# Performance work log

Measured on AMD Instinct MI355X. Metric: run time of the kernel, lower is better.

## Reference

```python
import jax, jax.numpy as jnp
import numpy as np

D_MODEL = 768
N_HEADS = 12
D_K = D_MODEL // N_HEADS
NEG_INF = -1e9


def setup_inputs() -> dict:
    key = jax.random.key(0)
    ks = jax.random.split(key, 7)
    B, S = 4, 2048
    x = jax.random.normal(ks[0], (B, S, D_MODEL), dtype=jnp.float32)
    # causal mask, broadcastable to [B, H, S, S]
    mask = jnp.tril(jnp.ones((S, S), dtype=bool))[None, None, :, :]
    scale = 1.0 / np.sqrt(D_MODEL)
    Wq = jax.random.normal(ks[1], (D_MODEL, D_MODEL), dtype=jnp.float32) * scale
    bq = jnp.zeros((D_MODEL,), dtype=jnp.float32)
    Wk = jax.random.normal(ks[2], (D_MODEL, D_MODEL), dtype=jnp.float32) * scale
    bk = jnp.zeros((D_MODEL,), dtype=jnp.float32)
    Wv = jax.random.normal(ks[3], (D_MODEL, D_MODEL), dtype=jnp.float32) * scale
    bv = jnp.zeros((D_MODEL,), dtype=jnp.float32)
    return {"x": x, "mask": mask, "Wq": Wq, "bq": bq, "Wk": Wk, "bk": bk, "Wv": Wv, "bv": bv}


def reference(x, mask, Wq, bq, Wk, bk, Wv, bv):
    B, S, _ = x.shape
    # projections (torch Linear: y = x @ W.T + b)
    q = (x @ Wq.T + bq).reshape(B, S, N_HEADS, D_K)
    k = (x @ Wk.T + bk).reshape(B, S, N_HEADS, D_K)
    v = (x @ Wv.T + bv).reshape(B, S, N_HEADS, D_K)
    # scores: [B, H, S, S]
    scores = jnp.einsum("bqhd,bkhd->bhqk", q, k) / jnp.sqrt(jnp.float32(D_K))
    scores = jnp.where(mask, scores, NEG_INF)
    probs = jax.nn.softmax(scores, axis=-1)
    # attention: [B, H, S, D_K] -> [B, S, d_model]
    attn = jnp.einsum("bhqk,bkhd->bqhd", probs, v).reshape(B, S, D_MODEL)
    return attn
```

## Files before the change

### kernel.cpp

```cpp
#include <hip/hip_runtime.h>
#include <math.h>


#define S_LEN 2048
#define BATCH 4
#define HEADS 12
#define DM 768
#define DK 64
#define BH (BATCH*HEADS)
#define MROWS (BATCH*S_LEN)
#define QSCALE 0.1803368801111244f

typedef __attribute__((ext_vector_type(8))) short short8;
typedef __attribute__((ext_vector_type(4))) float floatx4;
typedef __attribute__((ext_vector_type(16))) float floatx16;
typedef __attribute__((ext_vector_type(4))) unsigned int uintx4;
typedef __attribute__((address_space(3))) unsigned char lds_byte;
typedef __attribute__((address_space(1))) const unsigned char glob_byte;

__device__ __forceinline__ unsigned short f2bf(float f) {
  union { float f; unsigned int u; } a; a.f = f;
  unsigned int u = a.u;
  return (unsigned short)((u + 0x7fffu + ((u >> 16) & 1u)) >> 16);
}

__global__ void cast_f32_bf16(const float* __restrict__ src,
                              unsigned short* __restrict__ dst, int n) {
  int i = (blockIdx.x * blockDim.x + threadIdx.x) * 4;
  if (i < n) {
    float4 v = *(const float4*)(src + i);
    ushort4 o;
    o.x = f2bf(v.x); o.y = f2bf(v.y); o.z = f2bf(v.z); o.w = f2bf(v.w);
    *(ushort4*)(dst + i) = o;
  }
}

__global__ void cast_w3(const float* __restrict__ w0, const float* __restrict__ w1,
                        const float* __restrict__ w2, unsigned short* __restrict__ dst,
                        int n) {
  const float* src = (blockIdx.y == 0) ? w0 : (blockIdx.y == 1) ? w1 : w2;
  int i = (blockIdx.x * blockDim.x + threadIdx.x) * 4;
  if (i < n) {
    float4 v = *(const float4*)(src + i);
    ushort4 o;
    o.x = f2bf(v.x); o.y = f2bf(v.y); o.z = f2bf(v.z); o.w = f2bf(v.w);
    *(ushort4*)(dst + (size_t)blockIdx.y * n + i) = o;
  }
}

__global__ __launch_bounds__(256) void qkv_gemm(
    const unsigned short* __restrict__ xb,
    const unsigned short* __restrict__ wb,
    const float* __restrict__ bq, const float* __restrict__ bk,
    const float* __restrict__ bv,
    unsigned short* __restrict__ qo,
    unsigned short* __restrict__ ko,
    unsigned short* __restrict__ vto) {
  __shared__ unsigned short a_lds[2 * 128 * 32];
  __shared__ unsigned short b_lds[2 * 128 * 32];
  const int mat = blockIdx.z;
  const int tid = threadIdx.x;
  const int wave = tid >> 6, lane = tid & 63, quad = lane >> 4, ln = lane & 15;
  const int wm = wave & 1, wn = wave >> 1;
  const int m_blk = blockIdx.x * 128, n_blk = blockIdx.y * 128;
  const unsigned short* w = wb + (size_t)mat * DM * DM;
  const int srow_i[2] = { (0 * 256 + wave * 64 + lane) >> 2,
                          (1 * 256 + wave * 64 + lane) >> 2 };
  const int sq = (lane & 3) * 8;

  const floatx4 fz = {0.f, 0.f, 0.f, 0.f};
  floatx4 acc[4][4];
#pragma unroll
  for (int mg = 0; mg < 4; mg++)
#pragma unroll
    for (int c = 0; c < 4; c++) acc[mg][c] = fz;

  for (int k0 = 0; k0 < DM; k0 += 64) {
#pragma unroll
    for (int p = 0; p < 2; p++)
#pragma unroll
      for (int i = 0; i < 2; i++) {
        const int cbase = i * 256 + wave * 64;
        const int row = srow_i[i];
        __builtin_amdgcn_global_load_lds(
            (glob_byte*)(xb + (size_t)(m_blk + row) * DM + k0 + p * 32 + sq),
            (lds_byte*)(a_lds + p * 4096 + cbase * 8), 16, 0, 0);
        __builtin_amdgcn_global_load_lds(
            (glob_byte*)(w + (size_t)(n_blk + row) * DM + k0 + p * 32 + sq),
            (lds_byte*)(b_lds + p * 4096 + cbase * 8), 16, 0, 0);
      }
    __syncthreads();

    short8 af[4][2], bf[4][2];
#pragma unroll
    for (int mg = 0; mg < 4; mg++)
#pragma unroll
      for (int p = 0; p < 2; p++)
        af[mg][p] = *(const short8*)(a_lds + p * 4096 + (wm * 64 + mg * 16 + ln) * 32 + quad * 8);
#pragma unroll
    for (int c = 0; c < 4; c++)
#pragma unroll
      for (int p = 0; p < 2; p++)
        bf[c][p] = *(const short8*)(b_lds + p * 4096 + (wn * 64 + c * 16 + ln) * 32 + quad * 8);
#pragma unroll
    for (int mg = 0; mg < 4; mg++)
#pragma unroll
      for (int c = 0; c < 4; c++) {
        acc[mg][c] = __builtin_amdgcn_mfma_f32_16x16x32_bf16(af[mg][0], bf[c][0], acc[mg][c], 0, 0, 0);
        acc[mg][c] = __builtin_amdgcn_mfma_f32_16x16x32_bf16(af[mg][1], bf[c][1], acc[mg][c], 0, 0, 0);
      }
    __syncthreads();
  }

  const float* bias = (mat == 0) ? bq : (mat == 1) ? bk : bv;
  const float oscale = (mat == 0) ? QSCALE : 1.0f;
  const int m_base = m_blk + wm * 64, n_base = n_blk + wn * 64;
#pragma unroll
  for (int mg = 0; mg < 4; mg++)
#pragma unroll
    for (int c = 0; c < 4; c++) {
      int gn = n_base + c * 16 + ln;
      int hd = gn >> 6, d = gn & 63;
      float bias_v = bias[gn] * oscale;
      int gm0 = m_base + mg * 16 + quad * 4;
      int bb = gm0 >> 11, s0 = gm0 & (S_LEN - 1);
      if (mat == 2) {
        ushort4 pk;
        pk.x = f2bf(acc[mg][c][0] + bias_v);
        pk.y = f2bf(acc[mg][c][1] + bias_v);
        pk.z = f2bf(acc[mg][c][2] + bias_v);
        pk.w = f2bf(acc[mg][c][3] + bias_v);
        *(ushort4*)(vto + (((size_t)(bb * HEADS + hd)) * DK + d) * S_LEN + s0) = pk;
      } else {
        unsigned short* dst = (mat == 0 ? qo : ko) +
            (((size_t)(bb * HEADS + hd)) * S_LEN + s0) * DK + d;
#pragma unroll
        for (int r = 0; r < 4; r++)
          dst[(size_t)r * DK] = f2bf(acc[mg][c][r] * oscale + bias_v);
      }
    }
}

__global__ __launch_bounds__(128) void flash_attn(
    const unsigned short* __restrict__ q,
    const unsigned short* __restrict__ k,
    const unsigned short* __restrict__ vt,
    float* __restrict__ out) {
  const int id = blockIdx.x;
  const int bh = id % BH;
  const int qt = (S_LEN / 64 - 1) - (id / BH);
  const int q0 = qt * 64;
  const int tid = threadIdx.x;
  const int wave = tid >> 6, lane = tid & 63;
  const int l31 = lane & 31, hi = lane >> 5;
  const unsigned short* qp = q  + (size_t)bh * S_LEN * DK;
  const unsigned short* kp = k  + (size_t)bh * S_LEN * DK;
  const unsigned short* vp = vt + (size_t)bh * DK * S_LEN;
  const int qr_base = q0 + wave * 32;

  const floatx16 fz16 = {0.f,0.f,0.f,0.f,0.f,0.f,0.f,0.f,
                         0.f,0.f,0.f,0.f,0.f,0.f,0.f,0.f};

  short8 ones;
#pragma unroll
  for (int j = 0; j < 8; j++) ones[j] = (short)0x3F80;

  short8 aq[4];
#pragma unroll
  for (int ks = 0; ks < 4; ks++)
    aq[ks] = *(const short8*)(qp + (size_t)(qr_base + l31) * DK + ks * 16 + hi * 8);

  floatx16 o0 = fz16, o1 = fz16, lacc = fz16;

  auto loadK = [&](int k0, short8 (&kf)[2][4]) {
#pragma unroll
    for (int kg = 0; kg < 2; kg++)
#pragma unroll
      for (int ks = 0; ks < 4; ks++)
        kf[kg][ks] = *(const short8*)(kp + (size_t)(k0 + kg * 32 + l31) * DK + ks * 16 + hi * 8);
  };

  auto body = [&](int k0, short8 (&kf)[2][4]) {
    short8 vf[2][2][2];
#pragma unroll
    for (int dg = 0; dg < 2; dg++)
#pragma unroll
      for (int kg = 0; kg < 2; kg++)
#pragma unroll
        for (int ks2 = 0; ks2 < 2; ks2++)
          vf[dg][kg][ks2] = *(const short8*)(vp + (size_t)(dg * 32 + l31) * S_LEN
                                             + k0 + kg * 32 + ks2 * 16 + hi * 8);
    const bool domask = (k0 + 63 > qr_base);
#pragma unroll
    for (int kg = 0; kg < 2; kg++) {
      floatx16 sc = fz16;
#pragma unroll
      for (int ks = 0; ks < 4; ks++)
        sc = __builtin_amdgcn_mfma_f32_32x32x16_bf16(kf[kg][ks], aq[ks], sc, 0, 0, 0);
      float pv[16];
      const int qr = qr_base + l31;
#pragma unroll
      for (int r = 0; r < 16; r++) {
        float e = exp2f(sc[r]);
        if (domask) {
          int key = k0 + kg * 32 + (r & 3) + 8 * (r >> 2) + 4 * hi;
          e = (key <= qr) ? e : 0.f;
        }
        pv[r] = e;
      }
      unsigned int dw[4][2];
#pragma unroll
      for (int b = 0; b < 4; b++)
#pragma unroll
        for (int c = 0; c < 2; c++)
          asm("v_cvt_pk_bf16_f32 %0, %1, %2"
              : "=v"(dw[b][c]) : "v"(pv[4 * b + 2 * c]), "v"(pv[4 * b + 2 * c + 1]));
#pragma unroll
      for (int ks2 = 0; ks2 < 2; ks2++) {
        unsigned int a0 = dw[2 * ks2][0], a1 = dw[2 * ks2][1];
        unsigned int b0 = dw[2 * ks2 + 1][0], b1 = dw[2 * ks2 + 1][1];
        asm("v_permlane32_swap_b32 %0, %1" : "+v"(a0), "+v"(b0));
        asm("v_permlane32_swap_b32 %0, %1" : "+v"(a1), "+v"(b1));
        union { uintx4 u; short8 s; } ap;
        ap.u = (uintx4){a0, a1, b0, b1};
        o0 = __builtin_amdgcn_mfma_f32_32x32x16_bf16(ap.s, vf[0][kg][ks2], o0, 0, 0, 0);
        o1 = __builtin_amdgcn_mfma_f32_32x32x16_bf16(ap.s, vf[1][kg][ks2], o1, 0, 0, 0);
        lacc = __builtin_amdgcn_mfma_f32_32x32x16_bf16(ap.s, ones, lacc, 0, 0, 0);
      }
    }
  };

  const int kend = qr_base + 32;
  short8 kfa[2][4], kfb[2][4];
  loadK(0, kfa);
  int k0 = 0;
  for (; k0 + 64 < kend; k0 += 128) {
    loadK(k0 + 64, kfb);
    body(k0, kfa);
    loadK(k0 + 128, kfa);
    body(k0 + 64, kfb);
  }
  if (k0 < kend) body(k0, kfa);

  const int b = bh / HEADS, hd = bh % HEADS;
#pragma unroll
  for (int r = 0; r < 16; r++) {
    float inv = 1.f / lacc[r];
    int qrow = qr_base + (r & 3) + 8 * (r >> 2) + 4 * hi;
    float* orow = out + ((size_t)(b * S_LEN + qrow)) * DM + hd * DK;
    orow[l31]      = o0[r] * inv;
    orow[32 + l31] = o1[r] * inv;
  }
}

extern "C" void kernel_launch(void* const* d_in, const int* in_sizes, int n_in,
                              void* d_out, int out_size, void* d_ws, size_t ws_size,
                              hipStream_t stream) {
  const float* x  = (const float*)d_in[0];
  const float* Wq = (const float*)d_in[2];
  const float* bq = (const float*)d_in[3];
  const float* Wk = (const float*)d_in[4];
  const float* bk = (const float*)d_in[5];
  const float* Wv = (const float*)d_in[6];
  const float* bv = (const float*)d_in[7];
  float* out = (float*)d_out;

  const int NX = MROWS * DM;
  const int NW = DM * DM;
  unsigned short* xb = (unsigned short*)d_ws;
  unsigned short* wb = xb + NX;
  unsigned short* qo = wb + 3 * NW;
  unsigned short* ko = qo + (size_t)BH * S_LEN * DK;
  unsigned short* vt = ko + (size_t)BH * S_LEN * DK;

  cast_f32_bf16<<<(NX / 4 + 255) / 256, 256, 0, stream>>>(x, xb, NX);
  cast_w3<<<dim3((NW / 4 + 255) / 256, 3), 256, 0, stream>>>(Wq, Wk, Wv, wb, NW);

  qkv_gemm<<<dim3(MROWS / 128, DM / 128, 3), 256, 0, stream>>>(
      xb, wb, bq, bk, bv, qo, ko, vt);

  flash_attn<<<dim3((S_LEN / 64) * BH), 128, 0, stream>>>(qo, ko, vt, out);
}
```

Before: 256.1 us.

## Split causal attention key range into two halves and combine partials

Each query tile's key range is split into two halves processed by separate blocks, which doubles the grid and shortens each block's critical path under causal imbalance. Each half writes unnormalised partial outputs and row sums to a workspace. A new elementwise kernel adds the two halves and divides by the combined sum. The cost is an extra full-size fp32 partial buffer written and read, plus one more kernel launch.

```diff
diff --git a/kernel.cpp b/kernel.cpp
--- a/kernel.cpp
+++ b/kernel.cpp
@@ -145,11 +145,16 @@
     const unsigned short* __restrict__ q,
     const unsigned short* __restrict__ k,
     const unsigned short* __restrict__ vt,
-    float* __restrict__ out) {
+    float* __restrict__ out,
+    float* __restrict__ po1,
+    float* __restrict__ pl) {
   const int id = blockIdx.x;
   const int bh = id % BH;
-  const int qt = (S_LEN / 64 - 1) - (id / BH);
+  const int rest = id / BH;
+  const int qt = (S_LEN / 64 - 1) - (rest >> 1);
+  const int half = rest & 1;
   const int q0 = qt * 64;
+  const int h = ((qt + 1) >> 1) * 64;
   const int tid = threadIdx.x;
   const int wave = tid >> 6, lane = tid & 63;
   const int l31 = lane & 31, hi = lane >> 5;
@@ -230,27 +235,55 @@
     }
   };
 
-  const int kend = qr_base + 32;
+  const int kend = half ? (qr_base + 32) : h;
+  const int kbeg = half ? h : 0;
   short8 kfa[2][4], kfb[2][4];
-  loadK(0, kfa);
-  int k0 = 0;
-  for (; k0 + 64 < kend; k0 += 128) {
-    loadK(k0 + 64, kfb);
-    body(k0, kfa);
-    loadK(k0 + 128, kfa);
-    body(k0 + 64, kfb);
-  }
-  if (k0 < kend) body(k0, kfa);
+  int k0 = kbeg;
+  if (k0 < kend) {
+    loadK(k0, kfa);
+    for (; k0 + 64 < kend; k0 += 128) {
+      loadK(k0 + 64, kfb);
+      body(k0, kfa);
+      loadK(k0 + 128, kfa);
+      body(k0 + 64, kfb);
+    }
+    if (k0 < kend) body(k0, kfa);
+  }
 
   const int b = bh / HEADS, hd = bh % HEADS;
+  float* obase = half ? po1 : out;
+  float* plh = pl + ((size_t)half * BH + bh) * S_LEN;
 #pragma unroll
   for (int r = 0; r < 16; r++) {
-    float inv = 1.f / lacc[r];
     int qrow = qr_base + (r & 3) + 8 * (r >> 2) + 4 * hi;
-    float* orow = out + ((size_t)(b * S_LEN + qrow)) * DM + hd * DK;
-    orow[l31]      = o0[r] * inv;
-    orow[32 + l31] = o1[r] * inv;
-  }
+    float* orow = obase + ((size_t)(b * S_LEN + qrow)) * DM + hd * DK;
+    orow[l31]      = o0[r];
+    orow[32 + l31] = o1[r];
+    if (l31 == 0) plh[qrow] = lacc[r];
+  }
+}
+
+__global__ __launch_bounds__(256) void combine_out(
+    const float* __restrict__ po1,
+    const float* __restrict__ pl,
+    float* __restrict__ out) {
+  size_t gid = (size_t)blockIdx.x * 256 + threadIdx.x;
+  size_t i4 = gid * 4;
+  int dm = (int)(i4 % DM);
+  size_t rowg = i4 / DM;
+  int b = (int)(rowg >> 11), s = (int)(rowg & (S_LEN - 1));
+  int hd = dm >> 6;
+  size_t lidx = (size_t)(b * HEADS + hd) * S_LEN + s;
+  float l = pl[lidx] + pl[(size_t)BH * S_LEN + lidx];
+  float rl = 1.f / l;
+  float4 a = *(const float4*)(out + i4);
+  float4 c = *(const float4*)(po1 + i4);
+  float4 o;
+  o.x = (a.x + c.x) * rl;
+  o.y = (a.y + c.y) * rl;
+  o.z = (a.z + c.z) * rl;
+  o.w = (a.w + c.w) * rl;
+  *(float4*)(out + i4) = o;
 }
 
 extern "C" void kernel_launch(void* const* d_in, const int* in_sizes, int n_in,
@@ -267,11 +300,14 @@
 
   const int NX = MROWS * DM;
   const int NW = DM * DM;
+  const size_t NQK = (size_t)BH * S_LEN * DK;
   unsigned short* xb = (unsigned short*)d_ws;
   unsigned short* wb = xb + NX;
   unsigned short* qo = wb + 3 * NW;
-  unsigned short* ko = qo + (size_t)BH * S_LEN * DK;
-  unsigned short* vt = ko + (size_t)BH * S_LEN * DK;
+  unsigned short* ko = qo + NQK;
+  unsigned short* vt = ko + NQK;
+  float* po1 = (float*)(vt + NQK);
+  float* pl  = po1 + (size_t)MROWS * DM;
 
   cast_f32_bf16<<<(NX / 4 + 255) / 256, 256, 0, stream>>>(x, xb, NX);
   cast_w3<<<dim3((NW / 4 + 255) / 256, 3), 256, 0, stream>>>(Wq, Wk, Wv, wb, NW);
@@ -279,5 +315,8 @@
   qkv_gemm<<<dim3(MROWS / 128, DM / 128, 3), 256, 0, stream>>>(
       xb, wb, bq, bk, bv, qo, ko, vt);
 
-  flash_attn<<<dim3((S_LEN / 64) * BH), 128, 0, stream>>>(qo, ko, vt, out);
-}
+  flash_attn<<<dim3(2 * (S_LEN / 64) * BH), 128, 0, stream>>>(
+      qo, ko, vt, out, po1, pl);
+
+  combine_out<<<(MROWS * DM / 4) / 256, 256, 0, stream>>>(po1, pl, out);
+}
```

Result: slower. 267.6 us (+4.5%).
